# Optimization experiments

Measured on AMD Instinct MI355X. Metric: run time of the kernel, lower is better.

Reference implementation:

```python
import jax, jax.numpy as jnp
import numpy as np

# dims: T tokens, H hidden, E experts, I expert intermediate, K top-k
T, H, E, I, K = 2048, 1024, 64, 768, 8


def setup_inputs() -> dict:
    key = jax.random.key(0)
    k0, k1, k2, k3, k4 = jax.random.split(key, 5)
    s = 0.02  # init scale
    return {
        "hidden_states": jax.random.normal(k0, (T, H), jnp.float32),
        "w_router": jax.random.normal(k1, (E, H), jnp.float32) * s,   # gate (router) Linear, no bias
        "w_gate": jax.random.normal(k2, (E, I, H), jnp.float32) * s,  # per-expert gate_proj (out,in)
        "w_up": jax.random.normal(k3, (E, I, H), jnp.float32) * s,    # per-expert up_proj
        "w_down": jax.random.normal(k4, (E, H, I), jnp.float32) * s,  # per-expert down_proj
    }


def reference(hidden_states, w_router, w_gate, w_up, w_down):
    x = hidden_states  # (T, H)
    # --- router: softmax scores, top-k selection, renormalize (select_experts, softmax scoring) ---
    router_logits = jnp.einsum("th,eh->te", x, w_router)          # (T, E)
    probs = jax.nn.softmax(router_logits, axis=-1)
    topk_w, topk_ids = jax.lax.top_k(probs, K)                     # (T, K)
    topk_w = topk_w / jnp.sum(topk_w, axis=-1, keepdims=True)      # renormalize=True
    # scatter per-slot weights into a (T, E) combine matrix (zero for unselected experts)
    route = jnp.zeros((x.shape[0], E), x.dtype)
    route = route.at[jnp.arange(x.shape[0])[:, None], topk_ids].add(topk_w)
    # --- experts: SwiGLU MLP per expert, weighted combine (FusedMoE dispatch/combine) ---
    g = jnp.einsum("th,eih->tei", x, w_gate)                       # (T, E, I)
    u = jnp.einsum("th,eih->tei", x, w_up)
    h = jax.nn.silu(g) * u
    y = jnp.einsum("tei,ehi,te->th", h, w_down, route)             # weighted scatter-combine
    return y
```

## Files before the change

### kernel.cpp

```cpp
#include <hip/hip_runtime.h>
#include <hip/hip_bf16.h>
#include <cstdint>
#include <cstddef>

#define T_TOK 2048
#define H_DIM 1024
#define E_NUM 64
#define I_DIM 768
#define K_TOP 8
#define BM 384

typedef __attribute__((ext_vector_type(8))) __bf16 bf16x8;
typedef __attribute__((ext_vector_type(4))) __bf16 bf16x4;
typedef __attribute__((ext_vector_type(8))) unsigned short u16x8;
typedef __attribute__((ext_vector_type(4))) float f32x4;
typedef unsigned short ushort_t;

__device__ __forceinline__ unsigned short f2bf(float f) {
  uint32_t u = __builtin_bit_cast(uint32_t, f);
  u += 0x7fffu + ((u >> 16) & 1u);
  return (unsigned short)(u >> 16);
}

__device__ __forceinline__ bf16x8 cvt8b(f32x4 a, f32x4 b) {
  bf16x8 r;
  r[0] = (__bf16)a[0]; r[1] = (__bf16)a[1]; r[2] = (__bf16)a[2]; r[3] = (__bf16)a[3];
  r[4] = (__bf16)b[0]; r[5] = (__bf16)b[1]; r[6] = (__bf16)b[2]; r[7] = (__bf16)b[3];
  return r;
}

__device__ __forceinline__ bf16x4 cvt4b(f32x4 a) {
  bf16x4 r;
  r[0] = (__bf16)a[0]; r[1] = (__bf16)a[1]; r[2] = (__bf16)a[2]; r[3] = (__bf16)a[3];
  return r;
}

__device__ __forceinline__ void async16(const void* l, const void* g) {
  __builtin_amdgcn_global_load_lds(
      (const __attribute__((address_space(1))) unsigned int*)g,
      (__attribute__((address_space(3))) unsigned int*)l, 16, 0, 0);
}

__global__ __launch_bounds__(256) void xcast_kernel(const float* __restrict__ x,
                                                    ushort_t* __restrict__ xb) {
  int i = blockIdx.x * 256 + threadIdx.x;
  const f32x4* s = (const f32x4*)(x + (size_t)i * 8);
  *(bf16x8*)(xb + (size_t)i * 8) = cvt8b(s[0], s[1]);
}

__global__ __launch_bounds__(64) void router_kernel(
    const float* __restrict__ x, const float* __restrict__ wr,
    int* __restrict__ topk_id, float* __restrict__ topk_w,
    int* __restrict__ counts) {
  const int t = blockIdx.x;
  const int e = threadIdx.x;
  const float4* xv = (const float4*)(x + (size_t)t * H_DIM);
  const float4* wv = (const float4*)(wr + (size_t)e * H_DIM);
  float acc = 0.f;
#pragma unroll 8
  for (int i = 0; i < H_DIM / 4; ++i) {
    float4 a = xv[i], b = wv[i];
    acc = fmaf(a.x, b.x, acc);
    acc = fmaf(a.y, b.y, acc);
    acc = fmaf(a.z, b.z, acc);
    acc = fmaf(a.w, b.w, acc);
  }
  float m = acc;
  for (int o = 32; o; o >>= 1) m = fmaxf(m, __shfl_xor(m, o));
  float p = __expf(acc - m);
  float s = p;
  for (int o = 32; o; o >>= 1) s += __shfl_xor(s, o);
  p /= s;
  float v = p;
  int sid = 0;
  float sw = 0.f;
  for (int k = 0; k < K_TOP; ++k) {
    float bv = v;
    int bi = e;
    for (int o = 32; o; o >>= 1) {
      float ov = __shfl_xor(bv, o);
      int oi = __shfl_xor(bi, o);
      if (ov > bv || (ov == bv && oi < bi)) { bv = ov; bi = oi; }
    }
    if (e == k) { sid = bi; sw = bv; }
    if (e == bi) v = -1.f;
  }
  float ssum = (e < K_TOP) ? sw : 0.f;
  for (int o = 32; o; o >>= 1) ssum += __shfl_xor(ssum, o);
  if (e < K_TOP) {
    topk_id[t * K_TOP + e] = sid;
    topk_w[t * K_TOP + e] = sw / ssum;
    atomicAdd(&counts[sid], 1);
  }
}

__global__ __launch_bounds__(64) void scan_kernel(
    const int* __restrict__ counts, int* __restrict__ offsets,
    int* __restrict__ cursor) {
  int e = threadIdx.x;
  int ne = counts[e];
  int x = ne;
  for (int o = 1; o < 64; o <<= 1) {
    int v = __shfl_up(x, o);
    if (e >= o) x += v;
  }
  int excl = x - ne;
  offsets[e] = excl;
  cursor[e] = excl;
}

__global__ __launch_bounds__(256) void build_kernel(
    const int* __restrict__ topk_id, const float* __restrict__ topk_w,
    int* __restrict__ cursor, int* __restrict__ pair_token, float* __restrict__ pair_w) {
  int i = blockIdx.x * 256 + threadIdx.x;
  int t = i >> 3;
  int e = topk_id[i];
  int pos = atomicAdd(&cursor[e], 1);
  pair_token[pos] = t;
  pair_w[pos] = topk_w[i];
}


#define GU_NIT 32

__global__ __launch_bounds__(768, 3) void gemm_gu_kernel(
    const ushort_t* __restrict__ xb, const float* __restrict__ wg,
    const float* __restrict__ wu, const int* __restrict__ offsets,
    const int* __restrict__ counts, const int* __restrict__ pair_token,
    ushort_t* __restrict__ h_buf) {
  int idx = (blockIdx.x & 7) * 96 + (blockIdx.x >> 3);
  int e = idx / 12, nt = idx - e * 12;
  int ne = counts[e], off = offsets[e];
  int ib = nt * 64;

  __shared__ __align__(16) ushort_t Xs[3][BM * 32];
  __shared__ __align__(16) ushort_t Gs[2][64 * 32];
  __shared__ __align__(16) ushort_t Us[2][64 * 32];
  __shared__ int sTok[BM];

  const int tid = threadIdx.x;
  const int lane = tid & 63;
  const int wid = tid >> 6;
  if (tid < BM) {
    sTok[tid] = pair_token[off + (tid < ne ? tid : ne - 1)];
  }
  __syncthreads();

  const ushort_t* xsrc[2];
#pragma unroll
  for (int j = 0; j < 2; ++j) {
    int p = j * 768 + tid;
    int row = p >> 2, c = p & 3;
    xsrc[j] = xb + (size_t)sTok[row] * H_DIM + ((c ^ ((row >> 1) & 3)) << 3);
  }
  const float* gsrc = wg;
  const float* usrc = wu;
  int wdsti = 0;
  if (wid < 8) {
    int wrow = tid >> 3, wq = tid & 7;
    size_t ro = ((size_t)e * I_DIM + ib + wrow) * H_DIM + wq * 4;
    gsrc = wg + ro;
    usrc = wu + ro;
    wdsti = wrow * 32 + (((wq >> 1) ^ ((wrow >> 1) & 3)) << 3) + ((wq & 1) << 2);
  }

  const int wrM = wid >> 1, wrN = wid & 1;
  const int lrow = lane & 15, lk = lane >> 4;
  const bool wact = (wrM * 64) < ne;

  f32x4 accG[4][2], accU[4][2];
#pragma unroll
  for (int mi = 0; mi < 4; ++mi)
#pragma unroll
    for (int ni = 0; ni < 2; ++ni) {
      accG[mi][ni] = f32x4{0.f, 0.f, 0.f, 0.f};
      accU[mi][ni] = f32x4{0.f, 0.f, 0.f, 0.f};
    }

  f32x4 g0 = {0, 0, 0, 0}, u0 = {0, 0, 0, 0}, g1 = {0, 0, 0, 0}, u1 = {0, 0, 0, 0};

#define GU_XDMA(XB, K0)                                            \
  do {                                                             \
    async16(&Xs[XB][(wid * 64) * 8], xsrc[0] + (K0));              \
    async16(&Xs[XB][(768 + wid * 64) * 8], xsrc[1] + (K0));        \
  } while (0)

#define GU_WAIT                                                             \
  do {                                                                      \
    if (wid < 8) asm volatile("s_waitcnt vmcnt(6)" ::: "memory");           \
    else         asm volatile("s_waitcnt vmcnt(4)" ::: "memory");           \
  } while (0)

#define GU_BODY(XB, WB)                                                                  \
  do {                                                                                   \
    if (wact) {                                                                          \
      __builtin_amdgcn_s_setprio(1);                                                     \
      bf16x8 af[4];                                                                      \
      _Pragma("unroll") for (int mi = 0; mi < 4; ++mi) {                                 \
        int r = wrM * 64 + mi * 16 + lrow;                                               \
        af[mi] = __builtin_bit_cast(                                                     \
            bf16x8, *(const u16x8*)&Xs[XB][r * 32 + ((lk ^ ((r >> 1) & 3)) << 3)]);      \
      }                                                                                  \
      _Pragma("unroll") for (int ni = 0; ni < 2; ++ni) {                                 \
        int br = wrN * 32 + ni * 16 + lrow;                                              \
        int ci = br * 32 + ((lk ^ ((br >> 1) & 3)) << 3);                                \
        bf16x8 bg = __builtin_bit_cast(bf16x8, *(const u16x8*)&Gs[WB][ci]);              \
        bf16x8 bu = __builtin_bit_cast(bf16x8, *(const u16x8*)&Us[WB][ci]);              \
        _Pragma("unroll") for (int mi = 0; mi < 4; ++mi) {                               \
          accG[mi][ni] =                                                                 \
              __builtin_amdgcn_mfma_f32_16x16x32_bf16(af[mi], bg, accG[mi][ni], 0, 0, 0);\
          accU[mi][ni] =                                                                 \
              __builtin_amdgcn_mfma_f32_16x16x32_bf16(af[mi], bu, accU[mi][ni], 0, 0, 0);\
        }                                                                                \
      }                                                                                  \
      __builtin_amdgcn_s_setprio(0);                                                     \
    }                                                                                    \
  } while (0)

#define GU_ITER(K, XB, GH, UH, GL, UL)                                   \
  do {                                                                   \
    if (wid < 8) {                                                       \
      int kw = ((K) + 2 < GU_NIT) ? ((K) + 2) * 32 : 0;                  \
      GL = *(const f32x4*)(gsrc + kw);                                   \
      UL = *(const f32x4*)(usrc + kw);                                   \
    }                                                                    \
    GU_BODY(XB, (K) & 1);                                                \
    __builtin_amdgcn_s_barrier();                                        \
    __builtin_amdgcn_sched_barrier(0);                                   \
    {                                                                    \
      int kx = ((K) + 3 < GU_NIT) ? ((K) + 3) * 32 : 0;                  \
      GU_XDMA(XB, kx);                                                   \
    }                                                                    \
    GU_WAIT;                                                             \
    __builtin_amdgcn_sched_barrier(0);                                   \
    if (wid < 8) {                                                       \
      *(bf16x4*)&Gs[((K) + 1) & 1][wdsti] = cvt4b(GH);                   \
      *(bf16x4*)&Us[((K) + 1) & 1][wdsti] = cvt4b(UH);                   \
    }                                                                    \
    asm volatile("s_waitcnt lgkmcnt(0)" ::: "memory");                   \
    __builtin_amdgcn_s_barrier();                                        \
    __builtin_amdgcn_sched_barrier(0);                                   \
  } while (0)

  GU_XDMA(0, 0);
  if (wid < 8) {
    g0 = *(const f32x4*)(gsrc);
    u0 = *(const f32x4*)(usrc);
  }
  GU_XDMA(1, 32);
  if (wid < 8) {
    g1 = *(const f32x4*)(gsrc + 32);
    u1 = *(const f32x4*)(usrc + 32);
  }
  GU_XDMA(2, 64);
  GU_WAIT;
  __builtin_amdgcn_sched_barrier(0);
  if (wid < 8) {
    *(bf16x4*)&Gs[0][wdsti] = cvt4b(g0);
    *(bf16x4*)&Us[0][wdsti] = cvt4b(u0);
  }
  asm volatile("s_waitcnt lgkmcnt(0)" ::: "memory");
  __builtin_amdgcn_s_barrier();
  __builtin_amdgcn_sched_barrier(0);

  int kk = 0;
#pragma unroll 1
  for (; kk + 6 <= GU_NIT - 2; kk += 6) {
    GU_ITER(kk + 0, 0, g1, u1, g0, u0);
    GU_ITER(kk + 1, 1, g0, u0, g1, u1);
    GU_ITER(kk + 2, 2, g1, u1, g0, u0);
    GU_ITER(kk + 3, 0, g0, u0, g1, u1);
    GU_ITER(kk + 4, 1, g1, u1, g0, u0);
    GU_ITER(kk + 5, 2, g0, u0, g1, u1);
  }
  GU_ITER(30, 0, g1, u1, g0, u0);
  GU_ITER(31, 1, g0, u0, g1, u1);
  asm volatile("s_waitcnt vmcnt(0)" ::: "memory");
#undef GU_ITER
#undef GU_BODY
#undef GU_WAIT
#undef GU_XDMA

#pragma unroll
  for (int mi = 0; mi < 4; ++mi)
#pragma unroll
    for (int ni = 0; ni < 2; ++ni)
#pragma unroll
      for (int r = 0; r < 4; ++r) {
        int grow = wrM * 64 + mi * 16 + lk * 4 + r;
        if (grow < ne) {
          int col = ib + wrN * 32 + ni * 16 + lrow;
          float g = accG[mi][ni][r], u = accU[mi][ni][r];
          float hv = g / (1.f + __expf(-g)) * u;
          h_buf[(size_t)(off + grow) * I_DIM + col] = f2bf(hv);
        }
      }
}

#define DN_NIT 24

__global__ __launch_bounds__(768, 3) void gemm_down_kernel(
    const ushort_t* __restrict__ h_buf, const float* __restrict__ wd,
    const int* __restrict__ offsets, const int* __restrict__ counts,
    const int* __restrict__ pair_token, const float* __restrict__ pair_w,
    float* __restrict__ y) {
  int idx = (blockIdx.x & 7) * 64 + (blockIdx.x >> 3);
  int e = idx >> 3, nt = idx & 7;
  int ne = counts[e], off = offsets[e];
  int hb = nt * 128;

  __shared__ __align__(16) ushort_t Ah[3][BM * 32];
  __shared__ __align__(16) ushort_t Bs[2][128 * 32];
  __shared__ int sTok[BM];
  __shared__ float sPw[BM];

  const int tid = threadIdx.x;
  const int lane = tid & 63;
  const int wid = tid >> 6;
  if (tid < BM) {
    int ix = off + (tid < ne ? tid : ne - 1);
    sTok[tid] = pair_token[ix];
    sPw[tid] = pair_w[ix];
  }
  __syncthreads();

  const ushort_t* asrc[2];
#pragma unroll
  for (int j = 0; j < 2; ++j) {
    int p = j * 768 + tid;
    int row = p >> 2, c = p & 3;
    int hr = off + (row < ne ? row : ne - 1);
    asrc[j] = h_buf + (size_t)hr * I_DIM + ((c ^ ((row >> 1) & 3)) << 3);
  }
  const float* bsrc[2] = {wd, wd};
  int bdsti[2] = {0, 0};
  {
    int p0 = (tid < 256) ? tid : (256 + tid);
    int row = p0 >> 3, q = p0 & 7;
    bsrc[0] = wd + ((size_t)e * H_DIM + hb + row) * I_DIM + q * 4;
    bdsti[0] = row * 32 + (((q >> 1) ^ ((row >> 1) & 3)) << 3) + ((q & 1) << 2);
    if (tid < 256) {
      int p1 = 256 + tid;
      int r1 = p1 >> 3, q1 = p1 & 7;
      bsrc[1] = wd + ((size_t)e * H_DIM + hb + r1) * I_DIM + q1 * 4;
      bdsti[1] = r1 * 32 + (((q1 >> 1) ^ ((r1 >> 1) & 3)) << 3) + ((q1 & 1) << 2);
    }
  }

  const int wrM = wid >> 1, wrN = wid & 1;
  const int lrow = lane & 15, lk = lane >> 4;
  const bool wact = (wrM * 64) < ne;

  f32x4 acc[4][4];
#pragma unroll
  for (int mi = 0; mi < 4; ++mi)
#pragma unroll
    for (int ni = 0; ni < 4; ++ni) acc[mi][ni] = f32x4{0.f, 0.f, 0.f, 0.f};

  f32x4 b0a = {0, 0, 0, 0}, b0b = {0, 0, 0, 0}, b1a = {0, 0, 0, 0}, b1b = {0, 0, 0, 0};

#define DN_ADMA(XB, K0)                                            \
  do {                                                             \
    async16(&Ah[XB][(wid * 64) * 8], asrc[0] + (K0));              \
    async16(&Ah[XB][(768 + wid * 64) * 8], asrc[1] + (K0));        \
  } while (0)

#define DN_LDB(RA, RB, K0)                                         \
  do {                                                             \
    RA = *(const f32x4*)(bsrc[0] + (K0));                          \
    if (wid < 4) RB = *(const f32x4*)(bsrc[1] + (K0));             \
  } while (0)

#define DN_STB(WB, RA, RB)                                         \
  do {                                                             \
    *(bf16x4*)&Bs[WB][bdsti[0]] = cvt4b(RA);                       \
    if (wid < 4) *(bf16x4*)&Bs[WB][bdsti[1]] = cvt4b(RB);          \
  } while (0)

#define DN_WAIT                                                             \
  do {                                                                      \
    if (wid < 4) asm volatile("s_waitcnt vmcnt(6)" ::: "memory");           \
    else         asm volatile("s_waitcnt vmcnt(5)" ::: "memory");           \
  } while (0)

#define DN_BODY(XB, WB)                                                                  \
  do {                                                                                   \
    if (wact) {                                                                          \
      __builtin_amdgcn_s_setprio(1);                                                     \
      bf16x8 af[4];                                                                      \
      _Pragma("unroll") for (int mi = 0; mi < 4; ++mi) {                                 \
        int r = wrM * 64 + mi * 16 + lrow;                                               \
        af[mi] = __builtin_bit_cast(                                                     \
            bf16x8, *(const u16x8*)&Ah[XB][r * 32 + ((lk ^ ((r >> 1) & 3)) << 3)]);      \
      }                                                                                  \
      _Pragma("unroll") for (int ni = 0; ni < 4; ++ni) {                                 \
        int br = wrN * 64 + ni * 16 + lrow;                                              \
        bf16x8 bb = __builtin_bit_cast(                                                  \
            bf16x8, *(const u16x8*)&Bs[WB][br * 32 + ((lk ^ ((br >> 1) & 3)) << 3)]);    \
        _Pragma("unroll") for (int mi = 0; mi < 4; ++mi)                                 \
            acc[mi][ni] =                                                                \
                __builtin_amdgcn_mfma_f32_16x16x32_bf16(af[mi], bb, acc[mi][ni], 0, 0, 0);\
      }                                                                                  \
      __builtin_amdgcn_s_setprio(0);                                                     \
    }                                                                                    \
  } while (0)

#define DN_ITER(K, XB, BHa, BHb, BLa, BLb)                               \
  do {                                                                   \
    {                                                                    \
      int kw = ((K) + 2 < DN_NIT) ? ((K) + 2) * 32 : 0;                  \
      DN_LDB(BLa, BLb, kw);                                              \
    }                                                                    \
    DN_BODY(XB, (K) & 1);                                                \
    __builtin_amdgcn_s_barrier();                                        \
    __builtin_amdgcn_sched_barrier(0);                                   \
    {                                                                    \
      int kx = ((K) + 3 < DN_NIT) ? ((K) + 3) * 32 : 0;                  \
      DN_ADMA(XB, kx);                                                   \
    }                                                                    \
    DN_WAIT;                                                             \
    __builtin_amdgcn_sched_barrier(0);                                   \
    DN_STB(((K) + 1) & 1, BHa, BHb);                                     \
    asm volatile("s_waitcnt lgkmcnt(0)" ::: "memory");                   \
    __builtin_amdgcn_s_barrier();                                        \
    __builtin_amdgcn_sched_barrier(0);                                   \
  } while (0)

  DN_ADMA(0, 0);
  DN_LDB(b0a, b0b, 0);
  DN_ADMA(1, 32);
  DN_LDB(b1a, b1b, 32);
  DN_ADMA(2, 64);
  DN_WAIT;
  __builtin_amdgcn_sched_barrier(0);
  DN_STB(0, b0a, b0b);
  asm volatile("s_waitcnt lgkmcnt(0)" ::: "memory");
  __builtin_amdgcn_s_barrier();
  __builtin_amdgcn_sched_barrier(0);

  int kk = 0;
#pragma unroll 1
  for (; kk + 6 <= DN_NIT; kk += 6) {
    DN_ITER(kk + 0, 0, b1a, b1b, b0a, b0b);
    DN_ITER(kk + 1, 1, b0a, b0b, b1a, b1b);
    DN_ITER(kk + 2, 2, b1a, b1b, b0a, b0b);
    DN_ITER(kk + 3, 0, b0a, b0b, b1a, b1b);
    DN_ITER(kk + 4, 1, b1a, b1b, b0a, b0b);
    DN_ITER(kk + 5, 2, b0a, b0b, b1a, b1b);
  }
  asm volatile("s_waitcnt vmcnt(0)" ::: "memory");
#undef DN_ITER
#undef DN_BODY
#undef DN_WAIT
#undef DN_STB
#undef DN_LDB
#undef DN_ADMA

#pragma unroll
  for (int mi = 0; mi < 4; ++mi)
#pragma unroll
    for (int ni = 0; ni < 4; ++ni)
#pragma unroll
      for (int r = 0; r < 4; ++r) {
        int grow = wrM * 64 + mi * 16 + lk * 4 + r;
        if (grow < ne) {
          int col = hb + wrN * 64 + ni * 16 + lrow;
          float val = acc[mi][ni][r] * sPw[grow];
          unsafeAtomicAdd(&y[(size_t)sTok[grow] * H_DIM + col], val);
        }
      }
}

extern "C" void kernel_launch(void* const* d_in, const int* in_sizes, int n_in,
                              void* d_out, int out_size, void* d_ws, size_t ws_size,
                              hipStream_t stream) {
  const float* x  = (const float*)d_in[0];
  const float* wr = (const float*)d_in[1];
  const float* wg = (const float*)d_in[2];
  const float* wu = (const float*)d_in[3];
  const float* wd = (const float*)d_in[4];
  float* y = (float*)d_out;

  char* ws = (char*)d_ws;
  int* counts    = (int*)(ws + 0);
  int* offsets   = (int*)(ws + 256);
  int* cursor    = (int*)(ws + 512);
  int*   topk_id    = (int*)(ws + 2048);
  float* topk_w     = (float*)(ws + 2048 + 1 * 65536);
  int*   pair_token = (int*)(ws + 2048 + 2 * 65536);
  float* pair_w     = (float*)(ws + 2048 + 3 * 65536);
  ushort_t* h_buf = (ushort_t*)(ws + 2048 + 4 * 65536);
  ushort_t* xb = (ushort_t*)(ws + 2048 + 4 * 65536 + (size_t)T_TOK * I_DIM * K_TOP * 2);

  hipMemsetAsync(counts, 0, 256, stream);
  hipMemsetAsync(y, 0, (size_t)T_TOK * H_DIM * sizeof(float), stream);

  xcast_kernel<<<(T_TOK * H_DIM / 8) / 256, 256, 0, stream>>>(x, xb);
  router_kernel<<<T_TOK, 64, 0, stream>>>(x, wr, topk_id, topk_w, counts);
  scan_kernel<<<1, 64, 0, stream>>>(counts, offsets, cursor);
  build_kernel<<<(T_TOK * K_TOP) / 256, 256, 0, stream>>>(topk_id, topk_w, cursor, pair_token, pair_w);
  gemm_gu_kernel<<<768, 768, 0, stream>>>(
      xb, wg, wu, offsets, counts, pair_token, h_buf);
  gemm_down_kernel<<<512, 768, 0, stream>>>(
      h_buf, wd, offsets, counts, pair_token, pair_w, y);
}
```

Before: 377.9 us.

## Simplify GEMM pipelines to double buffering and batch router over four tokens

The router kernel now handles four tokens per block, reusing each weight load across four dot products and launching a quarter as many blocks. Both expert GEMM kernels move from a three-stage LDS ring with per-wave vmcnt waits to a plain double-buffered loop with a full vmcnt(0) wait each iteration. The down-proj B-tile load is rebalanced so the first eight waves each load two slices. The simpler pipeline frees LDS and may fit more blocks per CU, but it exposes more global-load latency since only one stage is in flight.

Result: no change. 372.7 us (median of 2 runs) (-1.4%).

```diff
diff --git a/kernel.cpp b/kernel.cpp
--- a/kernel.cpp
+++ b/kernel.cpp
@@ -52,45 +52,55 @@
     const float* __restrict__ x, const float* __restrict__ wr,
     int* __restrict__ topk_id, float* __restrict__ topk_w,
     int* __restrict__ counts) {
-  const int t = blockIdx.x;
+  const int t0 = blockIdx.x * 4;
   const int e = threadIdx.x;
-  const float4* xv = (const float4*)(x + (size_t)t * H_DIM);
   const float4* wv = (const float4*)(wr + (size_t)e * H_DIM);
-  float acc = 0.f;
-#pragma unroll 8
+  const float4* xv0 = (const float4*)(x + (size_t)t0 * H_DIM);
+  const float4* xv1 = (const float4*)(x + (size_t)(t0 + 1) * H_DIM);
+  const float4* xv2 = (const float4*)(x + (size_t)(t0 + 2) * H_DIM);
+  const float4* xv3 = (const float4*)(x + (size_t)(t0 + 3) * H_DIM);
+  float acc0 = 0.f, acc1 = 0.f, acc2 = 0.f, acc3 = 0.f;
+#pragma unroll 4
   for (int i = 0; i < H_DIM / 4; ++i) {
-    float4 a = xv[i], b = wv[i];
-    acc = fmaf(a.x, b.x, acc);
-    acc = fmaf(a.y, b.y, acc);
-    acc = fmaf(a.z, b.z, acc);
-    acc = fmaf(a.w, b.w, acc);
-  }
-  float m = acc;
-  for (int o = 32; o; o >>= 1) m = fmaxf(m, __shfl_xor(m, o));
-  float p = __expf(acc - m);
-  float s = p;
-  for (int o = 32; o; o >>= 1) s += __shfl_xor(s, o);
-  p /= s;
-  float v = p;
-  int sid = 0;
-  float sw = 0.f;
-  for (int k = 0; k < K_TOP; ++k) {
-    float bv = v;
-    int bi = e;
-    for (int o = 32; o; o >>= 1) {
-      float ov = __shfl_xor(bv, o);
-      int oi = __shfl_xor(bi, o);
-      if (ov > bv || (ov == bv && oi < bi)) { bv = ov; bi = oi; }
-    }
-    if (e == k) { sid = bi; sw = bv; }
-    if (e == bi) v = -1.f;
-  }
-  float ssum = (e < K_TOP) ? sw : 0.f;
-  for (int o = 32; o; o >>= 1) ssum += __shfl_xor(ssum, o);
-  if (e < K_TOP) {
-    topk_id[t * K_TOP + e] = sid;
-    topk_w[t * K_TOP + e] = sw / ssum;
-    atomicAdd(&counts[sid], 1);
+    float4 b = wv[i];
+    float4 a0 = xv0[i], a1 = xv1[i], a2 = xv2[i], a3 = xv3[i];
+    acc0 = fmaf(a0.x, b.x, fmaf(a0.y, b.y, fmaf(a0.z, b.z, fmaf(a0.w, b.w, acc0))));
+    acc1 = fmaf(a1.x, b.x, fmaf(a1.y, b.y, fmaf(a1.z, b.z, fmaf(a1.w, b.w, acc1))));
+    acc2 = fmaf(a2.x, b.x, fmaf(a2.y, b.y, fmaf(a2.z, b.z, fmaf(a2.w, b.w, acc2))));
+    acc3 = fmaf(a3.x, b.x, fmaf(a3.y, b.y, fmaf(a3.z, b.z, fmaf(a3.w, b.w, acc3))));
+  }
+  float accs[4] = {acc0, acc1, acc2, acc3};
+#pragma unroll 1
+  for (int tt = 0; tt < 4; ++tt) {
+    int t = t0 + tt;
+    float acc = accs[tt];
+    float m = acc;
+    for (int o = 32; o; o >>= 1) m = fmaxf(m, __shfl_xor(m, o));
+    float p = __expf(acc - m);
+    float s = p;
+    for (int o = 32; o; o >>= 1) s += __shfl_xor(s, o);
+    p /= s;
+    float v = p;
+    int sid = 0;
+    float sw = 0.f;
+    for (int k = 0; k < K_TOP; ++k) {
+      float bv = v;
+      int bi = e;
+      for (int o = 32; o; o >>= 1) {
+        float ov = __shfl_xor(bv, o);
+        int oi = __shfl_xor(bi, o);
+        if (ov > bv || (ov == bv && oi < bi)) { bv = ov; bi = oi; }
+      }
+      if (e == k) { sid = bi; sw = bv; }
+      if (e == bi) v = -1.f;
+    }
+    float ssum = (e < K_TOP) ? sw : 0.f;
+    for (int o = 32; o; o >>= 1) ssum += __shfl_xor(ssum, o);
+    if (e < K_TOP) {
+      topk_id[t * K_TOP + e] = sid;
+      topk_w[t * K_TOP + e] = sw / ssum;
+      atomicAdd(&counts[sid], 1);
+    }
   }
 }
 
@@ -133,7 +143,7 @@
   int ne = counts[e], off = offsets[e];
   int ib = nt * 64;
 
-  __shared__ __align__(16) ushort_t Xs[3][BM * 32];
+  __shared__ __align__(16) ushort_t Xs[2][BM * 32];
   __shared__ __align__(16) ushort_t Gs[2][64 * 32];
   __shared__ __align__(16) ushort_t Us[2][64 * 32];
   __shared__ int sTok[BM];
@@ -177,108 +187,72 @@
       accU[mi][ni] = f32x4{0.f, 0.f, 0.f, 0.f};
     }
 
-  f32x4 g0 = {0, 0, 0, 0}, u0 = {0, 0, 0, 0}, g1 = {0, 0, 0, 0}, u1 = {0, 0, 0, 0};
-
-#define GU_XDMA(XB, K0)                                            \
+  f32x4 gA = {0, 0, 0, 0}, uA = {0, 0, 0, 0};
+
+#define GU_XDMA(B, K0)                                             \
   do {                                                             \
-    async16(&Xs[XB][(wid * 64) * 8], xsrc[0] + (K0));              \
-    async16(&Xs[XB][(768 + wid * 64) * 8], xsrc[1] + (K0));        \
+    async16(&Xs[B][(wid * 64) * 8], xsrc[0] + (K0));               \
+    async16(&Xs[B][(768 + wid * 64) * 8], xsrc[1] + (K0));         \
   } while (0)
 
-#define GU_WAIT                                                             \
-  do {                                                                      \
-    if (wid < 8) asm volatile("s_waitcnt vmcnt(6)" ::: "memory");           \
-    else         asm volatile("s_waitcnt vmcnt(4)" ::: "memory");           \
-  } while (0)
-
-#define GU_BODY(XB, WB)                                                                  \
-  do {                                                                                   \
-    if (wact) {                                                                          \
-      __builtin_amdgcn_s_setprio(1);                                                     \
-      bf16x8 af[4];                                                                      \
-      _Pragma("unroll") for (int mi = 0; mi < 4; ++mi) {                                 \
-        int r = wrM * 64 + mi * 16 + lrow;                                               \
-        af[mi] = __builtin_bit_cast(                                                     \
-            bf16x8, *(const u16x8*)&Xs[XB][r * 32 + ((lk ^ ((r >> 1) & 3)) << 3)]);      \
-      }                                                                                  \
-      _Pragma("unroll") for (int ni = 0; ni < 2; ++ni) {                                 \
-        int br = wrN * 32 + ni * 16 + lrow;                                              \
-        int ci = br * 32 + ((lk ^ ((br >> 1) & 3)) << 3);                                \
-        bf16x8 bg = __builtin_bit_cast(bf16x8, *(const u16x8*)&Gs[WB][ci]);              \
-        bf16x8 bu = __builtin_bit_cast(bf16x8, *(const u16x8*)&Us[WB][ci]);              \
-        _Pragma("unroll") for (int mi = 0; mi < 4; ++mi) {                               \
-          accG[mi][ni] =                                                                 \
-              __builtin_amdgcn_mfma_f32_16x16x32_bf16(af[mi], bg, accG[mi][ni], 0, 0, 0);\
-          accU[mi][ni] =                                                                 \
-              __builtin_amdgcn_mfma_f32_16x16x32_bf16(af[mi], bu, accU[mi][ni], 0, 0, 0);\
-        }                                                                                \
-      }                                                                                  \
-      __builtin_amdgcn_s_setprio(0);                                                     \
-    }                                                                                    \
-  } while (0)
-
-#define GU_ITER(K, XB, GH, UH, GL, UL)                                   \
-  do {                                                                   \
-    if (wid < 8) {                                                       \
-      int kw = ((K) + 2 < GU_NIT) ? ((K) + 2) * 32 : 0;                  \
-      GL = *(const f32x4*)(gsrc + kw);                                   \
-      UL = *(const f32x4*)(usrc + kw);                                   \
-    }                                                                    \
-    GU_BODY(XB, (K) & 1);                                                \
-    __builtin_amdgcn_s_barrier();                                        \
-    __builtin_amdgcn_sched_barrier(0);                                   \
-    {                                                                    \
-      int kx = ((K) + 3 < GU_NIT) ? ((K) + 3) * 32 : 0;                  \
-      GU_XDMA(XB, kx);                                                   \
-    }                                                                    \
-    GU_WAIT;                                                             \
-    __builtin_amdgcn_sched_barrier(0);                                   \
-    if (wid < 8) {                                                       \
-      *(bf16x4*)&Gs[((K) + 1) & 1][wdsti] = cvt4b(GH);                   \
-      *(bf16x4*)&Us[((K) + 1) & 1][wdsti] = cvt4b(UH);                   \
-    }                                                                    \
-    asm volatile("s_waitcnt lgkmcnt(0)" ::: "memory");                   \
-    __builtin_amdgcn_s_barrier();                                        \
-    __builtin_amdgcn_sched_barrier(0);                                   \
-  } while (0)
-
   GU_XDMA(0, 0);
   if (wid < 8) {
-    g0 = *(const f32x4*)(gsrc);
-    u0 = *(const f32x4*)(usrc);
-  }
-  GU_XDMA(1, 32);
-  if (wid < 8) {
-    g1 = *(const f32x4*)(gsrc + 32);
-    u1 = *(const f32x4*)(usrc + 32);
-  }
-  GU_XDMA(2, 64);
-  GU_WAIT;
+    gA = *(const f32x4*)(gsrc);
+    uA = *(const f32x4*)(usrc);
+  }
+  asm volatile("s_waitcnt vmcnt(0)" ::: "memory");
   __builtin_amdgcn_sched_barrier(0);
   if (wid < 8) {
-    *(bf16x4*)&Gs[0][wdsti] = cvt4b(g0);
-    *(bf16x4*)&Us[0][wdsti] = cvt4b(u0);
+    *(bf16x4*)&Gs[0][wdsti] = cvt4b(gA);
+    *(bf16x4*)&Us[0][wdsti] = cvt4b(uA);
   }
   asm volatile("s_waitcnt lgkmcnt(0)" ::: "memory");
   __builtin_amdgcn_s_barrier();
   __builtin_amdgcn_sched_barrier(0);
 
-  int kk = 0;
-#pragma unroll 1
-  for (; kk + 6 <= GU_NIT - 2; kk += 6) {
-    GU_ITER(kk + 0, 0, g1, u1, g0, u0);
-    GU_ITER(kk + 1, 1, g0, u0, g1, u1);
-    GU_ITER(kk + 2, 2, g1, u1, g0, u0);
-    GU_ITER(kk + 3, 0, g0, u0, g1, u1);
-    GU_ITER(kk + 4, 1, g1, u1, g0, u0);
-    GU_ITER(kk + 5, 2, g0, u0, g1, u1);
-  }
-  GU_ITER(30, 0, g1, u1, g0, u0);
-  GU_ITER(31, 1, g0, u0, g1, u1);
-  asm volatile("s_waitcnt vmcnt(0)" ::: "memory");
-#undef GU_ITER
-#undef GU_BODY
-#undef GU_WAIT
+#pragma unroll 2
+  for (int K = 0; K < GU_NIT; ++K) {
+    const int B = K & 1;
+    if (K + 1 < GU_NIT) {
+      GU_XDMA(B ^ 1, (K + 1) * 32);
+      if (wid < 8) {
+        gA = *(const f32x4*)(gsrc + (K + 1) * 32);
+        uA = *(const f32x4*)(usrc + (K + 1) * 32);
+      }
+    }
+    if (wact) {
+      __builtin_amdgcn_s_setprio(1);
+      bf16x8 af[4];
+#pragma unroll
+      for (int mi = 0; mi < 4; ++mi) {
+        int r = wrM * 64 + mi * 16 + lrow;
+        af[mi] = __builtin_bit_cast(
+            bf16x8, *(const u16x8*)&Xs[B][r * 32 + ((lk ^ ((r >> 1) & 3)) << 3)]);
+      }
+#pragma unroll
+      for (int ni = 0; ni < 2; ++ni) {
+        int br = wrN * 32 + ni * 16 + lrow;
+        int ci = br * 32 + ((lk ^ ((br >> 1) & 3)) << 3);
+        bf16x8 bg = __builtin_bit_cast(bf16x8, *(const u16x8*)&Gs[B][ci]);
+        bf16x8 bu = __builtin_bit_cast(bf16x8, *(const u16x8*)&Us[B][ci]);
+#pragma unroll
+        for (int mi = 0; mi < 4; ++mi) {
+          accG[mi][ni] = __builtin_amdgcn_mfma_f32_16x16x32_bf16(af[mi], bg, accG[mi][ni], 0, 0, 0);
+          accU[mi][ni] = __builtin_amdgcn_mfma_f32_16x16x32_bf16(af[mi], bu, accU[mi][ni], 0, 0, 0);
+        }
+      }
+      __builtin_amdgcn_s_setprio(0);
+    }
+    asm volatile("s_waitcnt vmcnt(0)" ::: "memory");
+    __builtin_amdgcn_sched_barrier(0);
+    if (K + 1 < GU_NIT && wid < 8) {
+      *(bf16x4*)&Gs[B ^ 1][wdsti] = cvt4b(gA);
+      *(bf16x4*)&Us[B ^ 1][wdsti] = cvt4b(uA);
+    }
+    asm volatile("s_waitcnt lgkmcnt(0)" ::: "memory");
+    __builtin_amdgcn_s_barrier();
+    __builtin_amdgcn_sched_barrier(0);
+  }
 #undef GU_XDMA
 
 #pragma unroll
@@ -309,7 +283,7 @@
   int ne = counts[e], off = offsets[e];
   int hb = nt * 128;
 
-  __shared__ __align__(16) ushort_t Ah[3][BM * 32];
+  __shared__ __align__(16) ushort_t Ah[2][BM * 32];
   __shared__ __align__(16) ushort_t Bs[2][128 * 32];
   __shared__ int sTok[BM];
   __shared__ float sPw[BM];
@@ -332,19 +306,17 @@
     int hr = off + (row < ne ? row : ne - 1);
     asrc[j] = h_buf + (size_t)hr * I_DIM + ((c ^ ((row >> 1) & 3)) << 3);
   }
-  const float* bsrc[2] = {wd, wd};
-  int bdsti[2] = {0, 0};
-  {
-    int p0 = (tid < 256) ? tid : (256 + tid);
-    int row = p0 >> 3, q = p0 & 7;
-    bsrc[0] = wd + ((size_t)e * H_DIM + hb + row) * I_DIM + q * 4;
-    bdsti[0] = row * 32 + (((q >> 1) ^ ((row >> 1) & 3)) << 3) + ((q & 1) << 2);
-    if (tid < 256) {
-      int p1 = 256 + tid;
-      int r1 = p1 >> 3, q1 = p1 & 7;
-      bsrc[1] = wd + ((size_t)e * H_DIM + hb + r1) * I_DIM + q1 * 4;
-      bdsti[1] = r1 * 32 + (((q1 >> 1) ^ ((r1 >> 1) & 3)) << 3) + ((q1 & 1) << 2);
-    }
+  const float* bsrc0 = wd;
+  const float* bsrc1 = wd;
+  int bdst0 = 0, bdst1 = 0;
+  if (wid < 8) {
+    int r0 = tid >> 3, q0 = tid & 7;
+    bsrc0 = wd + ((size_t)e * H_DIM + hb + r0) * I_DIM + q0 * 4;
+    bdst0 = r0 * 32 + (((q0 >> 1) ^ ((r0 >> 1) & 3)) << 3) + ((q0 & 1) << 2);
+    int p1 = 512 + tid;
+    int r1 = p1 >> 3, q1 = p1 & 7;
+    bsrc1 = wd + ((size_t)e * H_DIM + hb + r1) * I_DIM + q1 * 4;
+    bdst1 = r1 * 32 + (((q1 >> 1) ^ ((r1 >> 1) & 3)) << 3) + ((q1 & 1) << 2);
   }
 
   const int wrM = wid >> 1, wrN = wid & 1;
@@ -357,103 +329,69 @@
 #pragma unroll
     for (int ni = 0; ni < 4; ++ni) acc[mi][ni] = f32x4{0.f, 0.f, 0.f, 0.f};
 
-  f32x4 b0a = {0, 0, 0, 0}, b0b = {0, 0, 0, 0}, b1a = {0, 0, 0, 0}, b1b = {0, 0, 0, 0};
-
-#define DN_ADMA(XB, K0)                                            \
+  f32x4 bA = {0, 0, 0, 0}, bB = {0, 0, 0, 0};
+
+#define DN_ADMA(B, K0)                                             \
   do {                                                             \
-    async16(&Ah[XB][(wid * 64) * 8], asrc[0] + (K0));              \
-    async16(&Ah[XB][(768 + wid * 64) * 8], asrc[1] + (K0));        \
+    async16(&Ah[B][(wid * 64) * 8], asrc[0] + (K0));               \
+    async16(&Ah[B][(768 + wid * 64) * 8], asrc[1] + (K0));         \
   } while (0)
 
-#define DN_LDB(RA, RB, K0)                                         \
-  do {                                                             \
-    RA = *(const f32x4*)(bsrc[0] + (K0));                          \
-    if (wid < 4) RB = *(const f32x4*)(bsrc[1] + (K0));             \
-  } while (0)
-
-#define DN_STB(WB, RA, RB)                                         \
-  do {                                                             \
-    *(bf16x4*)&Bs[WB][bdsti[0]] = cvt4b(RA);                       \
-    if (wid < 4) *(bf16x4*)&Bs[WB][bdsti[1]] = cvt4b(RB);          \
-  } while (0)
-
-#define DN_WAIT                                                             \
-  do {                                                                      \
-    if (wid < 4) asm volatile("s_waitcnt vmcnt(6)" ::: "memory");           \
-    else         asm volatile("s_waitcnt vmcnt(5)" ::: "memory");           \
-  } while (0)
-
-#define DN_BODY(XB, WB)                                                                  \
-  do {                                                                                   \
-    if (wact) {                                                                          \
-      __builtin_amdgcn_s_setprio(1);                                                     \
-      bf16x8 af[4];                                                                      \
-      _Pragma("unroll") for (int mi = 0; mi < 4; ++mi) {                                 \
-        int r = wrM * 64 + mi * 16 + lrow;                                               \
-        af[mi] = __builtin_bit_cast(                                                     \
-            bf16x8, *(const u16x8*)&Ah[XB][r * 32 + ((lk ^ ((r >> 1) & 3)) << 3)]);      \
-      }                                                                                  \
-      _Pragma("unroll") for (int ni = 0; ni < 4; ++ni) {                                 \
-        int br = wrN * 64 + ni * 16 + lrow;                                              \
-        bf16x8 bb = __builtin_bit_cast(                                                  \
-            bf16x8, *(const u16x8*)&Bs[WB][br * 32 + ((lk ^ ((br >> 1) & 3)) << 3)]);    \
-        _Pragma("unroll") for (int mi = 0; mi < 4; ++mi)                                 \
-            acc[mi][ni] =                                                                \
-                __builtin_amdgcn_mfma_f32_16x16x32_bf16(af[mi], bb, acc[mi][ni], 0, 0, 0);\
-      }                                                                                  \
-      __builtin_amdgcn_s_setprio(0);                                                     \
-    }                                                                                    \
-  } while (0)
-
-#define DN_ITER(K, XB, BHa, BHb, BLa, BLb)                               \
-  do {                                                                   \
-    {                                                                    \
-      int kw = ((K) + 2 < DN_NIT) ? ((K) + 2) * 32 : 0;                  \
-      DN_LDB(BLa, BLb, kw);                                              \
-    }                                                                    \
-    DN_BODY(XB, (K) & 1);                                                \
-    __builtin_amdgcn_s_barrier();                                        \
-    __builtin_amdgcn_sched_barrier(0);                                   \
-    {                                                                    \
-      int kx = ((K) + 3 < DN_NIT) ? ((K) + 3) * 32 : 0;                  \
-      DN_ADMA(XB, kx);                                                   \
-    }                                                                    \
-    DN_WAIT;                                                             \
-    __builtin_amdgcn_sched_barrier(0);                                   \
-    DN_STB(((K) + 1) & 1, BHa, BHb);                                     \
-    asm volatile("s_waitcnt lgkmcnt(0)" ::: "memory");                   \
-    __builtin_amdgcn_s_barrier();                                        \
-    __builtin_amdgcn_sched_barrier(0);                                   \
-  } while (0)
-
   DN_ADMA(0, 0);
-  DN_LDB(b0a, b0b, 0);
-  DN_ADMA(1, 32);
-  DN_LDB(b1a, b1b, 32);
-  DN_ADMA(2, 64);
-  DN_WAIT;
+  if (wid < 8) {
+    bA = *(const f32x4*)(bsrc0);
+    bB = *(const f32x4*)(bsrc1);
+  }
+  asm volatile("s_waitcnt vmcnt(0)" ::: "memory");
   __builtin_amdgcn_sched_barrier(0);
-  DN_STB(0, b0a, b0b);
+  if (wid < 8) {
+    *(bf16x4*)&Bs[0][bdst0] = cvt4b(bA);
+    *(bf16x4*)&Bs[0][bdst1] = cvt4b(bB);
+  }
   asm volatile("s_waitcnt lgkmcnt(0)" ::: "memory");
   __builtin_amdgcn_s_barrier();
   __builtin_amdgcn_sched_barrier(0);
 
-  int kk = 0;
-#pragma unroll 1
-  for (; kk + 6 <= DN_NIT; kk += 6) {
-    DN_ITER(kk + 0, 0, b1a, b1b, b0a, b0b);
-    DN_ITER(kk + 1, 1, b0a, b0b, b1a, b1b);
-    DN_ITER(kk + 2, 2, b1a, b1b, b0a, b0b);
-    DN_ITER(kk + 3, 0, b0a, b0b, b1a, b1b);
-    DN_ITER(kk + 4, 1, b1a, b1b, b0a, b0b);
-    DN_ITER(kk + 5, 2, b0a, b0b, b1a, b1b);
-  }
-  asm volatile("s_waitcnt vmcnt(0)" ::: "memory");
-#undef DN_ITER
-#undef DN_BODY
-#undef DN_WAIT
-#undef DN_STB
-#undef DN_LDB
+#pragma unroll 2
+  for (int K = 0; K < DN_NIT; ++K) {
+    const int B = K & 1;
+    if (K + 1 < DN_NIT) {
+      DN_ADMA(B ^ 1, (K + 1) * 32);
+      if (wid < 8) {
+        bA = *(const f32x4*)(bsrc0 + (K + 1) * 32);
+        bB = *(const f32x4*)(bsrc1 + (K + 1) * 32);
+      }
+    }
+    if (wact) {
+      __builtin_amdgcn_s_setprio(1);
+      bf16x8 af[4];
+#pragma unroll
+      for (int mi = 0; mi < 4; ++mi) {
+        int r = wrM * 64 + mi * 16 + lrow;
+        af[mi] = __builtin_bit_cast(
+            bf16x8, *(const u16x8*)&Ah[B][r * 32 + ((lk ^ ((r >> 1) & 3)) << 3)]);
+      }
+#pragma unroll
+      for (int ni = 0; ni < 4; ++ni) {
+        int br = wrN * 64 + ni * 16 + lrow;
+        bf16x8 bb = __builtin_bit_cast(
+            bf16x8, *(const u16x8*)&Bs[B][br * 32 + ((lk ^ ((br >> 1) & 3)) << 3)]);
+#pragma unroll
+        for (int mi = 0; mi < 4; ++mi)
+          acc[mi][ni] = __builtin_amdgcn_mfma_f32_16x16x32_bf16(af[mi], bb, acc[mi][ni], 0, 0, 0);
+      }
+      __builtin_amdgcn_s_setprio(0);
+    }
+    asm volatile("s_waitcnt vmcnt(0)" ::: "memory");
+    __builtin_amdgcn_sched_barrier(0);
+    if (K + 1 < DN_NIT && wid < 8) {
+      *(bf16x4*)&Bs[B ^ 1][bdst0] = cvt4b(bA);
+      *(bf16x4*)&Bs[B ^ 1][bdst1] = cvt4b(bB);
+    }
+    asm volatile("s_waitcnt lgkmcnt(0)" ::: "memory");
+    __builtin_amdgcn_s_barrier();
+    __builtin_amdgcn_sched_barrier(0);
+  }
 #undef DN_ADMA
 
 #pragma unroll
@@ -496,7 +434,7 @@
   hipMemsetAsync(y, 0, (size_t)T_TOK * H_DIM * sizeof(float), stream);
 
   xcast_kernel<<<(T_TOK * H_DIM / 8) / 256, 256, 0, stream>>>(x, xb);
-  router_kernel<<<T_TOK, 64, 0, stream>>>(x, wr, topk_id, topk_w, counts);
+  router_kernel<<<T_TOK / 4, 64, 0, stream>>>(x, wr, topk_id, topk_w, counts);
   scan_kernel<<<1, 64, 0, stream>>>(counts, offsets, cursor);
   build_kernel<<<(T_TOK * K_TOP) / 256, 256, 0, stream>>>(topk_id, topk_w, cursor, pair_token, pair_w);
   gemm_gu_kernel<<<768, 768, 0, stream>>>(
```
